# Kernel optimization log

Measured on AMD Instinct MI355X. Metric: run time of the kernel, lower is better.

## Reference

```python
import jax, jax.numpy as jnp
import numpy as np

N_NODES = 50000

def _gcn_layer(x, src, dst, W, b, n_nodes):
    # x: [N, F_in]; src/dst: [E+N] (self-loops already appended)
    h = x @ W  # [N, F_out]
    deg = jax.ops.segment_sum(jnp.ones_like(dst, dtype=h.dtype), dst, num_segments=n_nodes)
    dinv = jnp.where(deg > 0, jax.lax.rsqrt(deg), 0.0)  # deg^{-1/2}
    norm = dinv[src] * dinv[dst]  # [E+N]
    msg = h[src] * norm[:, None]  # gather + scale
    out = jax.ops.segment_sum(msg, dst, num_segments=n_nodes)  # scatter-add
    return out + b

def setup_inputs() -> dict:
    key = jax.random.key(0)
    k1, k2, k3, k4 = jax.random.split(key, 4)
    d = 128
    E = 800000
    x = jax.random.normal(k1, (N_NODES, d), dtype=jnp.float32)
    edge_index = jax.random.randint(k2, (2, E), 0, N_NODES, dtype=jnp.int64)
    W1 = jax.random.normal(k3, (d, d), dtype=jnp.float32) / np.sqrt(d)
    b1 = jnp.zeros((d,), dtype=jnp.float32)
    W2 = jax.random.normal(k4, (d, d), dtype=jnp.float32) / np.sqrt(d)
    b2 = jnp.zeros((d,), dtype=jnp.float32)
    return {"x": x, "edge_index": edge_index, "W1": W1, "b1": b1, "W2": W2, "b2": b2}

def reference(x, edge_index, W1, b1, W2, b2):
    n = x.shape[0]
    loops = jnp.arange(n, dtype=edge_index.dtype)
    src = jnp.concatenate([edge_index[0], loops])  # add self-loops
    dst = jnp.concatenate([edge_index[1], loops])
    h = _gcn_layer(x, src, dst, W1, b1, n)
    h = jax.nn.relu(h)
    z = _gcn_layer(h, src, dst, W2, b2, n)
    return z
```

## Files before the change

kernel.cpp:

```cpp
#include <hip/hip_runtime.h>
#include <hip/hip_fp16.h>

#define NF 128
#define KC 64
#define NPART 4
#define NPMAX 12544

typedef _Float16 half8  __attribute__((ext_vector_type(8)));
typedef _Float16 half4v __attribute__((ext_vector_type(4)));
typedef float    floatx4 __attribute__((ext_vector_type(4)));

__global__ __launch_bounds__(512) void count2_k(
    const int* __restrict__ dst, unsigned char* __restrict__ pcnt,
    int E, int N, int Ec)
{
    __shared__ int lcnt[NPMAX];
    const int p = blockIdx.x & 3, c = blockIdx.x >> 2;
    const int Np = (N + 3) >> 2;
    const int lo = p * Np, hi = min(lo + Np, N);
    const int sz = hi - lo;
    for (int i = threadIdx.x; i < sz; i += 512) lcnt[i] = 0;
    __syncthreads();

    const int e0 = c * Ec, e1 = min(e0 + Ec, E);
    for (int e = e0 + (int)threadIdx.x * 4; e + 3 < e1; e += 512 * 4) {
        int4 d = *(const int4*)(dst + e);
        if (d.x >= lo && d.x < hi) atomicAdd(&lcnt[d.x - lo], 1);
        if (d.y >= lo && d.y < hi) atomicAdd(&lcnt[d.y - lo], 1);
        if (d.z >= lo && d.z < hi) atomicAdd(&lcnt[d.z - lo], 1);
        if (d.w >= lo && d.w < hi) atomicAdd(&lcnt[d.w - lo], 1);
    }
    int rem0 = e0 + ((e1 - e0) & ~3);
    for (int e = rem0 + (int)threadIdx.x; e < e1; e += 512) {
        int d = dst[e];
        if (d >= lo && d < hi) atomicAdd(&lcnt[d - lo], 1);
    }
    __syncthreads();
    for (int i = threadIdx.x; i < sz; i += 512)
        pcnt[(size_t)c * N + lo + i] = (unsigned char)lcnt[i];
}

__global__ __launch_bounds__(256) void pscan2_k(
    unsigned char* __restrict__ pcnt, float* __restrict__ dinv,
    int* __restrict__ rowptr, int* __restrict__ blocksum, int n, int N, int nb,
    const float* __restrict__ W1, const float* __restrict__ W2,
    __half* __restrict__ WT1, __half* __restrict__ WT2)
{
    if ((int)blockIdx.x >= nb) {
        int idx = ((int)blockIdx.x - nb) * 256 + threadIdx.x;
        const float* W = (idx < 16384) ? W1 : W2;
        __half* WT     = (idx < 16384) ? WT1 : WT2;
        int j = idx & 16383;
        int nn = j & 127, k = j >> 7;
        WT[nn * NF + k] = __float2half(W[k * NF + nn]);
        return;
    }
    __shared__ int sm[256];
    int tid = threadIdx.x;
    int bin = blockIdx.x * 256 + tid;
    int total = 0;
    if (bin < n) {
        #pragma unroll 4
        for (int c = 0; c < KC; c++) {
            size_t o = (size_t)c * N + bin;
            int v = pcnt[o];
            pcnt[o] = (unsigned char)total;
            total += v;
        }
        dinv[bin] = rsqrtf((float)total + 1.0f);
    }
    sm[tid] = total;
    __syncthreads();
    #pragma unroll
    for (int d = 1; d < 256; d <<= 1) {
        int t = (tid >= d) ? sm[tid - d] : 0;
        __syncthreads();
        sm[tid] += t;
        __syncthreads();
    }
    if (bin < n) rowptr[bin] = sm[tid] - total;
    if (tid == 255) blocksum[blockIdx.x] = sm[255];
}

template<bool F32IN>
__device__ __forceinline__ void gemm_body512(
    const void* __restrict__ Xv, const __half* __restrict__ WT,
    const float* __restrict__ dinv, __half* __restrict__ out, int M, int bid,
    __half (*wlds)[136])
{
    const int tid = threadIdx.x;
    {
        int r = tid >> 2;
        int c0 = (tid & 3) * 32;
        const half8* s = (const half8*)(WT + (size_t)r * NF + c0);
        half8* d = (half8*)&wlds[r][c0];
        #pragma unroll
        for (int j = 0; j < 4; j++) d[j] = s[j];
    }
    __syncthreads();

    const int wave = tid >> 6, lane = tid & 63;
    const int quad = lane >> 4, l15 = lane & 15;
    const int rowA = bid * 128 + wave * 16 + l15;
    const int rowc = (rowA < M) ? rowA : (M - 1);

    half8 afr[4];
    if (F32IN) {
        const float* X = (const float*)Xv;
        #pragma unroll
        for (int kc = 0; kc < 4; kc++) {
            const floatx4* p = (const floatx4*)(X + (size_t)rowc * NF + kc * 32 + quad * 8);
            floatx4 u = p[0], v = p[1];
            half8 a;
            a[0] = (_Float16)u[0]; a[1] = (_Float16)u[1];
            a[2] = (_Float16)u[2]; a[3] = (_Float16)u[3];
            a[4] = (_Float16)v[0]; a[5] = (_Float16)v[1];
            a[6] = (_Float16)v[2]; a[7] = (_Float16)v[3];
            afr[kc] = a;
        }
    } else {
        const __half* X = (const __half*)Xv;
        #pragma unroll
        for (int kc = 0; kc < 4; kc++)
            afr[kc] = *(const half8*)(X + (size_t)rowc * NF + kc * 32 + quad * 8);
    }

    floatx4 acc[8];
    #pragma unroll
    for (int ct = 0; ct < 8; ct++) { floatx4 z = {0.f, 0.f, 0.f, 0.f}; acc[ct] = z; }

    #pragma unroll
    for (int kc = 0; kc < 4; kc++) {
        #pragma unroll
        for (int ct = 0; ct < 8; ct++) {
            half8 b = *(const half8*)&wlds[ct * 16 + l15][kc * 32 + quad * 8];
            acc[ct] = __builtin_amdgcn_mfma_f32_16x16x32_f16(afr[kc], b, acc[ct], 0, 0, 0);
        }
    }

    const int orow0 = bid * 128 + wave * 16 + quad * 4;
    #pragma unroll
    for (int r = 0; r < 4; r++) {
        int orow = orow0 + r;
        if (orow < M) {
            float s = dinv[orow];
            #pragma unroll
            for (int ct = 0; ct < 8; ct++)
                out[(size_t)orow * NF + ct * 16 + l15] = __float2half(acc[ct][r] * s);
        }
    }
}

__global__ __launch_bounds__(512) void mid_k(
    const int* __restrict__ src, const int* __restrict__ dst,
    const int* __restrict__ rowptr, const unsigned char* __restrict__ coff,
    const int* __restrict__ blocksum, int* __restrict__ rowptr2,
    int* __restrict__ csr, int E, int N, int Ec, int nb,
    const float* __restrict__ X, const __half* __restrict__ WT,
    const float* __restrict__ dinv, __half* __restrict__ H, int GB2)
{
    __shared__ __align__(16) char smem[NPMAX * 4 + 1024];
    const int tid = threadIdx.x;
    if ((int)blockIdx.x < GB2) {
        gemm_body512<true>(X, WT, dinv, H, N, blockIdx.x, (__half(*)[136])smem);
        return;
    }
    int* lcur = (int*)smem;
    int* pref = (int*)(smem + NPMAX * 4);

    const int b = blockIdx.x - GB2;
    const int p = b & 3, c = b >> 2;
    const int Np = (N + 3) >> 2;
    const int lo = p * Np, hi = min(lo + Np, N);
    const int sz = hi - lo;

    int v = (tid < nb) ? blocksum[tid] : 0;
    if (tid < 256) pref[tid] = v;
    __syncthreads();
    #pragma unroll
    for (int d = 1; d < 256; d <<= 1) {
        int t = (tid < 256 && tid >= d) ? pref[tid - d] : 0;
        __syncthreads();
        if (tid < 256) pref[tid] += t;
        __syncthreads();
    }
    if (tid < 256) pref[tid] -= v;
    __syncthreads();

    for (int i = tid; i < sz; i += 512) {
        int bin = lo + i;
        int r = rowptr[bin] + pref[bin >> 8] + (int)coff[(size_t)c * N + bin];
        lcur[i] = r;
        if (c == 0) rowptr2[bin] = r;
    }
    if (c == 0 && p == 0 && tid == 0) rowptr2[N] = E;
    __syncthreads();

    const int e0 = c * Ec, e1 = min(e0 + Ec, E);
    for (int e = e0 + tid * 4; e + 3 < e1; e += 512 * 4) {
        int4 d = *(const int4*)(dst + e);
        int4 s = *(const int4*)(src + e);
        if (d.x >= lo && d.x < hi) csr[atomicAdd(&lcur[d.x - lo], 1)] = s.x;
        if (d.y >= lo && d.y < hi) csr[atomicAdd(&lcur[d.y - lo], 1)] = s.y;
        if (d.z >= lo && d.z < hi) csr[atomicAdd(&lcur[d.z - lo], 1)] = s.z;
        if (d.w >= lo && d.w < hi) csr[atomicAdd(&lcur[d.w - lo], 1)] = s.w;
    }
    int rem0 = e0 + ((e1 - e0) & ~3);
    for (int e = rem0 + tid; e < e1; e += 512) {
        int d = dst[e];
        if (d >= lo && d < hi) csr[atomicAdd(&lcur[d - lo], 1)] = src[e];
    }
}

__device__ __forceinline__ void gather2w(
    const half8* __restrict__ hs8, const int* __restrict__ csr,
    const int* __restrict__ rowptr, int nA, int n,
    int g, int fl, int lane, floatx4& ac0, floatx4& ac1)
{
    const int ep  = g & 1;
    const int isB = g >> 1;
    const int nB  = nA + 1;

    int baseA = 0, cntA = 0, baseB = 0, cntB = 0;
    if (nA < n) {
        baseA = rowptr[nA];
        int mid = rowptr[nA + 1];
        cntA = mid - baseA;
        if (nB < n) { baseB = mid; cntB = rowptr[nB + 1] - mid; }
    }
    const int ccA = min(cntA, 64), ccB = min(cntB, 64);

    int idxA = (lane < ccA) ? __builtin_nontemporal_load(&csr[baseA + lane]) : 0;
    int idxB = (lane < ccB) ? __builtin_nontemporal_load(&csr[baseB + lane]) : 0;

    if (ep == 0) {
        int nd = isB ? nB : nA;
        if (nd < n) {
            half8 s = hs8[(size_t)nd * 16 + fl];
            ac0[0] += (float)s[0]; ac0[1] += (float)s[1];
            ac0[2] += (float)s[2]; ac0[3] += (float)s[3];
            ac1[0] += (float)s[4]; ac1[1] += (float)s[5];
            ac1[2] += (float)s[6]; ac1[3] += (float)s[7];
        }
    }

    const int myc  = isB ? ccB : ccA;
    const int maxc = max(ccA, ccB);
    for (int j = 0; j < maxc; j += 16) {
        int s[8];
        half8 v[8];
        #pragma unroll
        for (int t = 0; t < 8; t++) {
            int e = j + 2 * t + ep;
            int eA = min(e, ccA - 1); eA = (eA < 0) ? 0 : eA;
            int eB = min(e, ccB - 1); eB = (eB < 0) ? 0 : eB;
            int sa = __shfl(idxA, eA, 64);
            int sb = __shfl(idxB, eB, 64);
            s[t] = isB ? sb : sa;
        }
        #pragma unroll
        for (int t = 0; t < 8; t++)
            v[t] = hs8[(size_t)s[t] * 16 + fl];
        #pragma unroll
        for (int t = 0; t < 8; t++) {
            if (j + 2 * t + ep < myc) {
                ac0[0] += (float)v[t][0]; ac0[1] += (float)v[t][1];
                ac0[2] += (float)v[t][2]; ac0[3] += (float)v[t][3];
                ac1[0] += (float)v[t][4]; ac1[1] += (float)v[t][5];
                ac1[2] += (float)v[t][6]; ac1[3] += (float)v[t][7];
            }
        }
    }

    const int cmax = max(cntA, cntB);
    for (int off = 64; off < cmax; off += 64) {
        int cA2 = cntA - off; cA2 = (cA2 < 0) ? 0 : min(cA2, 64);
        int cB2 = cntB - off; cB2 = (cB2 < 0) ? 0 : min(cB2, 64);
        int iA2 = (lane < cA2) ? csr[baseA + off + lane] : 0;
        int iB2 = (lane < cB2) ? csr[baseB + off + lane] : 0;
        int myc2 = isB ? cB2 : cA2;
        int m2   = max(cA2, cB2);
        for (int j = 0; j < m2; j += 16) {
            int s[8];
            half8 v[8];
            #pragma unroll
            for (int t = 0; t < 8; t++) {
                int e = j + 2 * t + ep;
                int eA = min(e, cA2 - 1); eA = (eA < 0) ? 0 : eA;
                int eB = min(e, cB2 - 1); eB = (eB < 0) ? 0 : eB;
                int sa = __shfl(iA2, eA, 64);
                int sb = __shfl(iB2, eB, 64);
                s[t] = isB ? sb : sa;
            }
            #pragma unroll
            for (int t = 0; t < 8; t++)
                v[t] = hs8[(size_t)s[t] * 16 + fl];
            #pragma unroll
            for (int t = 0; t < 8; t++) {
                if (j + 2 * t + ep < myc2) {
                    ac0[0] += (float)v[t][0]; ac0[1] += (float)v[t][1];
                    ac0[2] += (float)v[t][2]; ac0[3] += (float)v[t][3];
                    ac1[0] += (float)v[t][4]; ac1[1] += (float)v[t][5];
                    ac1[2] += (float)v[t][6]; ac1[3] += (float)v[t][7];
                }
            }
        }
    }

    #pragma unroll
    for (int q = 0; q < 4; q++) {
        ac0[q] += __shfl_xor(ac0[q], 16, 64);
        ac1[q] += __shfl_xor(ac1[q], 16, 64);
    }
}

__global__ __launch_bounds__(512) void aggmm_k(
    const __half* __restrict__ hs, const int* __restrict__ rowptr,
    const int* __restrict__ csr, const float* __restrict__ dinv,
    const float* __restrict__ bias, const __half* __restrict__ WT,
    __half* __restrict__ Hout, int n)
{
    __shared__ __half alds[16][136];
    const int tid = threadIdx.x;
    const int wave = tid >> 6, lane = tid & 63;
    const int g = lane >> 4, fl = lane & 15;
    const int nb0 = blockIdx.x * 16;
    const int nA = nb0 + wave * 2;

    floatx4 ac0 = {0.f, 0.f, 0.f, 0.f}, ac1 = {0.f, 0.f, 0.f, 0.f};
    gather2w((const half8*)hs, csr, rowptr, nA, n, g, fl, lane, ac0, ac1);

    if ((g & 1) == 0) {
        int node = nA + (g >> 1);
        int row  = wave * 2 + (g >> 1);
        half8 hv;
        if (node < n) {
            float dv = dinv[node];
            const floatx4 bv0 = *(const floatx4*)&bias[fl * 8];
            const floatx4 bv1 = *(const floatx4*)&bias[fl * 8 + 4];
            hv[0] = (_Float16)fmaxf(dv * ac0[0] + bv0[0], 0.f);
            hv[1] = (_Float16)fmaxf(dv * ac0[1] + bv0[1], 0.f);
            hv[2] = (_Float16)fmaxf(dv * ac0[2] + bv0[2], 0.f);
            hv[3] = (_Float16)fmaxf(dv * ac0[3] + bv0[3], 0.f);
            hv[4] = (_Float16)fmaxf(dv * ac1[0] + bv1[0], 0.f);
            hv[5] = (_Float16)fmaxf(dv * ac1[1] + bv1[1], 0.f);
            hv[6] = (_Float16)fmaxf(dv * ac1[2] + bv1[2], 0.f);
            hv[7] = (_Float16)fmaxf(dv * ac1[3] + bv1[3], 0.f);
        } else {
            #pragma unroll
            for (int i = 0; i < 8; i++) hv[i] = (_Float16)0.f;
        }
        *(half8*)&alds[row][fl * 8] = hv;
    }
    __syncthreads();

    const int quad = lane >> 4, l15 = lane & 15;
    const int ct = wave;
    half8 afr[4];
    #pragma unroll
    for (int kc = 0; kc < 4; kc++)
        afr[kc] = *(const half8*)&alds[l15][kc * 32 + quad * 8];

    floatx4 o0 = {0.f, 0.f, 0.f, 0.f};
    #pragma unroll
    for (int kc = 0; kc < 4; kc++) {
        half8 b = *(const half8*)(WT + (size_t)(ct * 16 + l15) * NF + kc * 32 + quad * 8);
        o0 = __builtin_amdgcn_mfma_f32_16x16x32_f16(afr[kc], b, o0, 0, 0, 0);
    }

    #pragma unroll
    for (int r = 0; r < 4; r++) {
        int node = nb0 + quad * 4 + r;
        if (node < n) {
            float s = dinv[node];
            Hout[(size_t)node * NF + ct * 16 + l15] = __float2half(o0[r] * s);
        }
    }
}

__global__ __launch_bounds__(256) void agg4_k(
    const __half* __restrict__ hs, const int* __restrict__ rowptr,
    const int* __restrict__ csr, const float* __restrict__ dinv,
    const float* __restrict__ bias, float* __restrict__ outf, int n)
{
    const int tid = threadIdx.x;
    const int wave = tid >> 6, lane = tid & 63;
    const int g = lane >> 4, fl = lane & 15;
    const int nA = blockIdx.x * 8 + wave * 2;
    if (nA >= n) return;

    floatx4 ac0 = {0.f, 0.f, 0.f, 0.f}, ac1 = {0.f, 0.f, 0.f, 0.f};
    gather2w((const half8*)hs, csr, rowptr, nA, n, g, fl, lane, ac0, ac1);

    if ((g & 1) == 0) {
        int node = nA + (g >> 1);
        if (node < n) {
            float dv = dinv[node];
            const floatx4 bv0 = *(const floatx4*)&bias[fl * 8];
            const floatx4 bv1 = *(const floatx4*)&bias[fl * 8 + 4];
            floatx4 w0, w1;
            w0[0] = dv * ac0[0] + bv0[0]; w0[1] = dv * ac0[1] + bv0[1];
            w0[2] = dv * ac0[2] + bv0[2]; w0[3] = dv * ac0[3] + bv0[3];
            w1[0] = dv * ac1[0] + bv1[0]; w1[1] = dv * ac1[1] + bv1[1];
            w1[2] = dv * ac1[2] + bv1[2]; w1[3] = dv * ac1[3] + bv1[3];
            *(floatx4*)(outf + (size_t)node * NF + fl * 8)     = w0;
            *(floatx4*)(outf + (size_t)node * NF + fl * 8 + 4) = w1;
        }
    }
}


extern "C" void kernel_launch(void* const* d_in, const int* in_sizes, int n_in,
                              void* d_out, int out_size, void* d_ws, size_t ws_size,
                              hipStream_t stream) {
    const float* x  = (const float*)d_in[0];
    const int*   ei = (const int*)d_in[1];
    const float* W1 = (const float*)d_in[2];
    const float* b1 = (const float*)d_in[3];
    const float* W2 = (const float*)d_in[4];
    const float* b2 = (const float*)d_in[5];
    float* out = (float*)d_out;

    const int N = in_sizes[0] / NF;
    const int E = in_sizes[1] / 2;
    const int* src = ei;
    const int* dst = ei + E;

    char* ws = (char*)d_ws;
    size_t off = 0;
    auto alloc = [&](size_t bytes) {
        void* p = ws + off;
        off += bytes;
        off = (off + 63) & ~(size_t)63;
        return p;
    };
    unsigned char* pcnt = (unsigned char*)alloc((size_t)KC * N);
    int*    rowptr  = (int*)alloc((size_t)(N + 1) * 4);
    int*    rowptr2 = (int*)alloc((size_t)(N + 1) * 4);
    int*    csr     = (int*)alloc((size_t)E * 4);
    float*  dinv    = (float*)alloc((size_t)N * 4);
    int*    bsum    = (int*)alloc((size_t)256 * 4);
    __half* WT1     = (__half*)alloc((size_t)NF * NF * 2);
    __half* WT2     = (__half*)alloc((size_t)NF * NF * 2);
    __half* H16     = (__half*)alloc((size_t)N * NF * 2);
    __half* A16     = (__half*)alloc((size_t)N * NF * 2);

    int nb  = (N + 255) / 256;
    int Ec  = (((E + KC - 1) / KC) + 3) & ~3;
    int GB2 = (N + 127) / 128;
    int fb  = (N + 15) / 16;
    int ab  = (N + 7) / 8;

    count2_k<<<KC * NPART, 512, 0, stream>>>(dst, pcnt, E, N, Ec);
    pscan2_k<<<nb + 128, 256, 0, stream>>>(pcnt, dinv, rowptr, bsum, N, N, nb,
                                           W1, W2, WT1, WT2);
    mid_k<<<GB2 + KC * NPART, 512, 0, stream>>>(src, dst, rowptr, pcnt, bsum,
                                                rowptr2, csr, E, N, Ec, nb,
                                                x, WT1, dinv, H16, GB2);
    aggmm_k<<<fb, 512, 0, stream>>>(H16, rowptr2, csr, dinv, b1, WT2, A16, N);
    agg4_k<<<ab, 256, 0, stream>>>(A16, rowptr2, csr, dinv, b2, out, N);
}
```

Baseline: 204.3 us.

## Replace counting-sort CSR build with fixed-width padded adjacency plus overflow list

Removes the partitioned count, prefix-scan and scatter kernels. Edges now go straight into a padded per-node adjacency of width 64 using global atomics, and any edges past that width go to an overflow list. Degree normalisation is recomputed from the count array instead of a stored dinv. This saves several launches and the scan passes, but adds contended global atomics, a large sparse array, and a linear scan of the overflow list in the aggregation kernels whenever overflow occurs. The GEMM no longer runs fused alongside the scatter, so it now runs after the fill.

```diff
diff --git a/kernel.cpp b/kernel.cpp
--- a/kernel.cpp
+++ b/kernel.cpp
@@ -2,92 +2,68 @@
 #include <hip/hip_fp16.h>
 
 #define NF 128
-#define KC 64
-#define NPART 4
-#define NPMAX 12544
+#define DMAX 64
 
 typedef _Float16 half8  __attribute__((ext_vector_type(8)));
 typedef _Float16 half4v __attribute__((ext_vector_type(4)));
 typedef float    floatx4 __attribute__((ext_vector_type(4)));
 
-__global__ __launch_bounds__(512) void count2_k(
-    const int* __restrict__ dst, unsigned char* __restrict__ pcnt,
-    int E, int N, int Ec)
-{
-    __shared__ int lcnt[NPMAX];
-    const int p = blockIdx.x & 3, c = blockIdx.x >> 2;
-    const int Np = (N + 3) >> 2;
-    const int lo = p * Np, hi = min(lo + Np, N);
-    const int sz = hi - lo;
-    for (int i = threadIdx.x; i < sz; i += 512) lcnt[i] = 0;
-    __syncthreads();
-
-    const int e0 = c * Ec, e1 = min(e0 + Ec, E);
-    for (int e = e0 + (int)threadIdx.x * 4; e + 3 < e1; e += 512 * 4) {
-        int4 d = *(const int4*)(dst + e);
-        if (d.x >= lo && d.x < hi) atomicAdd(&lcnt[d.x - lo], 1);
-        if (d.y >= lo && d.y < hi) atomicAdd(&lcnt[d.y - lo], 1);
-        if (d.z >= lo && d.z < hi) atomicAdd(&lcnt[d.z - lo], 1);
-        if (d.w >= lo && d.w < hi) atomicAdd(&lcnt[d.w - lo], 1);
-    }
-    int rem0 = e0 + ((e1 - e0) & ~3);
-    for (int e = rem0 + (int)threadIdx.x; e < e1; e += 512) {
-        int d = dst[e];
-        if (d >= lo && d < hi) atomicAdd(&lcnt[d - lo], 1);
-    }
-    __syncthreads();
-    for (int i = threadIdx.x; i < sz; i += 512)
-        pcnt[(size_t)c * N + lo + i] = (unsigned char)lcnt[i];
-}
-
-__global__ __launch_bounds__(256) void pscan2_k(
-    unsigned char* __restrict__ pcnt, float* __restrict__ dinv,
-    int* __restrict__ rowptr, int* __restrict__ blocksum, int n, int N, int nb,
+__global__ __launch_bounds__(256) void z_k(
+    int* __restrict__ cnt, int N, int zb,
     const float* __restrict__ W1, const float* __restrict__ W2,
     __half* __restrict__ WT1, __half* __restrict__ WT2)
 {
-    if ((int)blockIdx.x >= nb) {
-        int idx = ((int)blockIdx.x - nb) * 256 + threadIdx.x;
-        const float* W = (idx < 16384) ? W1 : W2;
-        __half* WT     = (idx < 16384) ? WT1 : WT2;
-        int j = idx & 16383;
-        int nn = j & 127, k = j >> 7;
-        WT[nn * NF + k] = __float2half(W[k * NF + nn]);
+    int b = blockIdx.x;
+    if (b < zb) {
+        int i = b * 256 + threadIdx.x;
+        if (i <= N) cnt[i] = 0;
         return;
     }
-    __shared__ int sm[256];
-    int tid = threadIdx.x;
-    int bin = blockIdx.x * 256 + tid;
-    int total = 0;
-    if (bin < n) {
-        #pragma unroll 4
-        for (int c = 0; c < KC; c++) {
-            size_t o = (size_t)c * N + bin;
-            int v = pcnt[o];
-            pcnt[o] = (unsigned char)total;
-            total += v;
-        }
-        dinv[bin] = rsqrtf((float)total + 1.0f);
-    }
-    sm[tid] = total;
-    __syncthreads();
-    #pragma unroll
-    for (int d = 1; d < 256; d <<= 1) {
-        int t = (tid >= d) ? sm[tid - d] : 0;
-        __syncthreads();
-        sm[tid] += t;
-        __syncthreads();
-    }
-    if (bin < n) rowptr[bin] = sm[tid] - total;
-    if (tid == 255) blocksum[blockIdx.x] = sm[255];
-}
-
-template<bool F32IN>
-__device__ __forceinline__ void gemm_body512(
-    const void* __restrict__ Xv, const __half* __restrict__ WT,
-    const float* __restrict__ dinv, __half* __restrict__ out, int M, int bid,
-    __half (*wlds)[136])
-{
+    int idx = (b - zb) * 256 + threadIdx.x;
+    const float* W = (idx < 16384) ? W1 : W2;
+    __half* WT     = (idx < 16384) ? WT1 : WT2;
+    int j = idx & 16383;
+    int nn = j & 127, k = j >> 7;
+    WT[nn * NF + k] = __float2half(W[k * NF + nn]);
+}
+
+__device__ __forceinline__ void fill_one(
+    int d, int s, int* __restrict__ cnt, int* __restrict__ csrF,
+    int* __restrict__ ovf, int N)
+{
+    int pos = atomicAdd(&cnt[d], 1);
+    if (pos < DMAX) {
+        csrF[(size_t)d * DMAX + pos] = s;
+    } else {
+        int o = atomicAdd(&cnt[N], 1);
+        ovf[2 * o] = d; ovf[2 * o + 1] = s;
+    }
+}
+
+__global__ __launch_bounds__(256) void fill_k(
+    const int* __restrict__ src, const int* __restrict__ dst,
+    int* __restrict__ cnt, int* __restrict__ csrF, int* __restrict__ ovf,
+    int E, int N)
+{
+    int i4 = (blockIdx.x * 256 + threadIdx.x) * 4;
+    if (i4 + 3 < E) {
+        int4 d = *(const int4*)(dst + i4);
+        int4 s = *(const int4*)(src + i4);
+        fill_one(d.x, s.x, cnt, csrF, ovf, N);
+        fill_one(d.y, s.y, cnt, csrF, ovf, N);
+        fill_one(d.z, s.z, cnt, csrF, ovf, N);
+        fill_one(d.w, s.w, cnt, csrF, ovf, N);
+    } else {
+        for (int e = i4; e < E; e++)
+            fill_one(dst[e], src[e], cnt, csrF, ovf, N);
+    }
+}
+
+__global__ __launch_bounds__(512) void gemm1_k(
+    const float* __restrict__ X, const __half* __restrict__ WT,
+    const int* __restrict__ cnt, __half* __restrict__ H, int M)
+{
+    __shared__ __half wlds[128][136];
     const int tid = threadIdx.x;
     {
         int r = tid >> 2;
@@ -101,28 +77,20 @@
 
     const int wave = tid >> 6, lane = tid & 63;
     const int quad = lane >> 4, l15 = lane & 15;
-    const int rowA = bid * 128 + wave * 16 + l15;
+    const int rowA = blockIdx.x * 128 + wave * 16 + l15;
     const int rowc = (rowA < M) ? rowA : (M - 1);
 
     half8 afr[4];
-    if (F32IN) {
-        const float* X = (const float*)Xv;
-        #pragma unroll
-        for (int kc = 0; kc < 4; kc++) {
-            const floatx4* p = (const floatx4*)(X + (size_t)rowc * NF + kc * 32 + quad * 8);
-            floatx4 u = p[0], v = p[1];
-            half8 a;
-            a[0] = (_Float16)u[0]; a[1] = (_Float16)u[1];
-            a[2] = (_Float16)u[2]; a[3] = (_Float16)u[3];
-            a[4] = (_Float16)v[0]; a[5] = (_Float16)v[1];
-            a[6] = (_Float16)v[2]; a[7] = (_Float16)v[3];
-            afr[kc] = a;
-        }
-    } else {
-        const __half* X = (const __half*)Xv;
-        #pragma unroll
-        for (int kc = 0; kc < 4; kc++)
-            afr[kc] = *(const half8*)(X + (size_t)rowc * NF + kc * 32 + quad * 8);
+    #pragma unroll
+    for (int kc = 0; kc < 4; kc++) {
+        const floatx4* p = (const floatx4*)(X + (size_t)rowc * NF + kc * 32 + quad * 8);
+        floatx4 u = p[0], v = p[1];
+        half8 a;
+        a[0] = (_Float16)u[0]; a[1] = (_Float16)u[1];
+        a[2] = (_Float16)u[2]; a[3] = (_Float16)u[3];
+        a[4] = (_Float16)v[0]; a[5] = (_Float16)v[1];
+        a[6] = (_Float16)v[2]; a[7] = (_Float16)v[3];
+        afr[kc] = a;
     }
 
     floatx4 acc[8];
@@ -138,100 +106,35 @@
         }
     }
 
-    const int orow0 = bid * 128 + wave * 16 + quad * 4;
+    const int orow0 = blockIdx.x * 128 + wave * 16 + quad * 4;
     #pragma unroll
     for (int r = 0; r < 4; r++) {
         int orow = orow0 + r;
         if (orow < M) {
-            float s = dinv[orow];
+            float dv = rsqrtf((float)cnt[orow] + 1.0f);
             #pragma unroll
             for (int ct = 0; ct < 8; ct++)
-                out[(size_t)orow * NF + ct * 16 + l15] = __float2half(acc[ct][r] * s);
-        }
-    }
-}
-
-__global__ __launch_bounds__(512) void mid_k(
-    const int* __restrict__ src, const int* __restrict__ dst,
-    const int* __restrict__ rowptr, const unsigned char* __restrict__ coff,
-    const int* __restrict__ blocksum, int* __restrict__ rowptr2,
-    int* __restrict__ csr, int E, int N, int Ec, int nb,
-    const float* __restrict__ X, const __half* __restrict__ WT,
-    const float* __restrict__ dinv, __half* __restrict__ H, int GB2)
-{
-    __shared__ __align__(16) char smem[NPMAX * 4 + 1024];
-    const int tid = threadIdx.x;
-    if ((int)blockIdx.x < GB2) {
-        gemm_body512<true>(X, WT, dinv, H, N, blockIdx.x, (__half(*)[136])smem);
-        return;
-    }
-    int* lcur = (int*)smem;
-    int* pref = (int*)(smem + NPMAX * 4);
-
-    const int b = blockIdx.x - GB2;
-    const int p = b & 3, c = b >> 2;
-    const int Np = (N + 3) >> 2;
-    const int lo = p * Np, hi = min(lo + Np, N);
-    const int sz = hi - lo;
-
-    int v = (tid < nb) ? blocksum[tid] : 0;
-    if (tid < 256) pref[tid] = v;
-    __syncthreads();
-    #pragma unroll
-    for (int d = 1; d < 256; d <<= 1) {
-        int t = (tid < 256 && tid >= d) ? pref[tid - d] : 0;
-        __syncthreads();
-        if (tid < 256) pref[tid] += t;
-        __syncthreads();
-    }
-    if (tid < 256) pref[tid] -= v;
-    __syncthreads();
-
-    for (int i = tid; i < sz; i += 512) {
-        int bin = lo + i;
-        int r = rowptr[bin] + pref[bin >> 8] + (int)coff[(size_t)c * N + bin];
-        lcur[i] = r;
-        if (c == 0) rowptr2[bin] = r;
-    }
-    if (c == 0 && p == 0 && tid == 0) rowptr2[N] = E;
-    __syncthreads();
-
-    const int e0 = c * Ec, e1 = min(e0 + Ec, E);
-    for (int e = e0 + tid * 4; e + 3 < e1; e += 512 * 4) {
-        int4 d = *(const int4*)(dst + e);
-        int4 s = *(const int4*)(src + e);
-        if (d.x >= lo && d.x < hi) csr[atomicAdd(&lcur[d.x - lo], 1)] = s.x;
-        if (d.y >= lo && d.y < hi) csr[atomicAdd(&lcur[d.y - lo], 1)] = s.y;
-        if (d.z >= lo && d.z < hi) csr[atomicAdd(&lcur[d.z - lo], 1)] = s.z;
-        if (d.w >= lo && d.w < hi) csr[atomicAdd(&lcur[d.w - lo], 1)] = s.w;
-    }
-    int rem0 = e0 + ((e1 - e0) & ~3);
-    for (int e = rem0 + tid; e < e1; e += 512) {
-        int d = dst[e];
-        if (d >= lo && d < hi) csr[atomicAdd(&lcur[d - lo], 1)] = src[e];
+                H[(size_t)orow * NF + ct * 16 + l15] = __float2half(acc[ct][r] * dv);
+        }
     }
 }
 
 __device__ __forceinline__ void gather2w(
-    const half8* __restrict__ hs8, const int* __restrict__ csr,
-    const int* __restrict__ rowptr, int nA, int n,
-    int g, int fl, int lane, floatx4& ac0, floatx4& ac1)
+    const half8* __restrict__ hs8, const int* __restrict__ csrF,
+    const int* __restrict__ cnt, int nA, int n,
+    int g, int fl, int lane, floatx4& ac0, floatx4& ac1,
+    const int* __restrict__ ovf, int novf)
 {
     const int ep  = g & 1;
     const int isB = g >> 1;
     const int nB  = nA + 1;
 
-    int baseA = 0, cntA = 0, baseB = 0, cntB = 0;
-    if (nA < n) {
-        baseA = rowptr[nA];
-        int mid = rowptr[nA + 1];
-        cntA = mid - baseA;
-        if (nB < n) { baseB = mid; cntB = rowptr[nB + 1] - mid; }
-    }
-    const int ccA = min(cntA, 64), ccB = min(cntB, 64);
-
-    int idxA = (lane < ccA) ? __builtin_nontemporal_load(&csr[baseA + lane]) : 0;
-    int idxB = (lane < ccB) ? __builtin_nontemporal_load(&csr[baseB + lane]) : 0;
+    int cntA = (nA < n) ? cnt[nA] : 0;
+    int cntB = (nB < n) ? cnt[nB] : 0;
+    const int ccA = min(cntA, DMAX), ccB = min(cntB, DMAX);
+
+    int idxA = (lane < ccA) ? __builtin_nontemporal_load(&csrF[(size_t)nA * DMAX + lane]) : 0;
+    int idxB = (lane < ccB) ? __builtin_nontemporal_load(&csrF[(size_t)nB * DMAX + lane]) : 0;
 
     if (ep == 0) {
         int nd = isB ? nB : nA;
@@ -272,37 +175,16 @@
         }
     }
 
-    const int cmax = max(cntA, cntB);
-    for (int off = 64; off < cmax; off += 64) {
-        int cA2 = cntA - off; cA2 = (cA2 < 0) ? 0 : min(cA2, 64);
-        int cB2 = cntB - off; cB2 = (cB2 < 0) ? 0 : min(cB2, 64);
-        int iA2 = (lane < cA2) ? csr[baseA + off + lane] : 0;
-        int iB2 = (lane < cB2) ? csr[baseB + off + lane] : 0;
-        int myc2 = isB ? cB2 : cA2;
-        int m2   = max(cA2, cB2);
-        for (int j = 0; j < m2; j += 16) {
-            int s[8];
-            half8 v[8];
-            #pragma unroll
-            for (int t = 0; t < 8; t++) {
-                int e = j + 2 * t + ep;
-                int eA = min(e, cA2 - 1); eA = (eA < 0) ? 0 : eA;
-                int eB = min(e, cB2 - 1); eB = (eB < 0) ? 0 : eB;
-                int sa = __shfl(iA2, eA, 64);
-                int sb = __shfl(iB2, eB, 64);
-                s[t] = isB ? sb : sa;
-            }
-            #pragma unroll
-            for (int t = 0; t < 8; t++)
-                v[t] = hs8[(size_t)s[t] * 16 + fl];
-            #pragma unroll
-            for (int t = 0; t < 8; t++) {
-                if (j + 2 * t + ep < myc2) {
-                    ac0[0] += (float)v[t][0]; ac0[1] += (float)v[t][1];
-                    ac0[2] += (float)v[t][2]; ac0[3] += (float)v[t][3];
-                    ac1[0] += (float)v[t][4]; ac1[1] += (float)v[t][5];
-                    ac1[2] += (float)v[t][6]; ac1[3] += (float)v[t][7];
-                }
+    if (novf > 0 && ep == 0) {
+        int myN = isB ? nB : nA;
+        for (int i = 0; i < novf; i++) {
+            int d = ovf[2 * i];
+            if (d == myN) {
+                half8 v = hs8[(size_t)ovf[2 * i + 1] * 16 + fl];
+                ac0[0] += (float)v[0]; ac0[1] += (float)v[1];
+                ac0[2] += (float)v[2]; ac0[3] += (float)v[3];
+                ac1[0] += (float)v[4]; ac1[1] += (float)v[5];
+                ac1[2] += (float)v[6]; ac1[3] += (float)v[7];
             }
         }
     }
@@ -315,10 +197,10 @@
 }
 
 __global__ __launch_bounds__(512) void aggmm_k(
-    const __half* __restrict__ hs, const int* __restrict__ rowptr,
-    const int* __restrict__ csr, const float* __restrict__ dinv,
-    const float* __restrict__ bias, const __half* __restrict__ WT,
-    __half* __restrict__ Hout, int n)
+    const __half* __restrict__ hs, const int* __restrict__ csrF,
+    const int* __restrict__ cnt, const float* __restrict__ bias,
+    const __half* __restrict__ WT, __half* __restrict__ Hout, int n,
+    const int* __restrict__ ovf)
 {
     __shared__ __half alds[16][136];
     const int tid = threadIdx.x;
@@ -326,16 +208,17 @@
     const int g = lane >> 4, fl = lane & 15;
     const int nb0 = blockIdx.x * 16;
     const int nA = nb0 + wave * 2;
+    const int novf = cnt[n];
 
     floatx4 ac0 = {0.f, 0.f, 0.f, 0.f}, ac1 = {0.f, 0.f, 0.f, 0.f};
-    gather2w((const half8*)hs, csr, rowptr, nA, n, g, fl, lane, ac0, ac1);
+    gather2w((const half8*)hs, csrF, cnt, nA, n, g, fl, lane, ac0, ac1, ovf, novf);
 
     if ((g & 1) == 0) {
         int node = nA + (g >> 1);
         int row  = wave * 2 + (g >> 1);
         half8 hv;
         if (node < n) {
-            float dv = dinv[node];
+            float dv = rsqrtf((float)cnt[node] + 1.0f);
             const floatx4 bv0 = *(const floatx4*)&bias[fl * 8];
             const floatx4 bv1 = *(const floatx4*)&bias[fl * 8 + 4];
             hv[0] = (_Float16)fmaxf(dv * ac0[0] + bv0[0], 0.f);
@@ -372,30 +255,31 @@
     for (int r = 0; r < 4; r++) {
         int node = nb0 + quad * 4 + r;
         if (node < n) {
-            float s = dinv[node];
-            Hout[(size_t)node * NF + ct * 16 + l15] = __float2half(o0[r] * s);
+            float dv = rsqrtf((float)cnt[node] + 1.0f);
+            Hout[(size_t)node * NF + ct * 16 + l15] = __float2half(o0[r] * dv);
         }
     }
 }
 
 __global__ __launch_bounds__(256) void agg4_k(
-    const __half* __restrict__ hs, const int* __restrict__ rowptr,
-    const int* __restrict__ csr, const float* __restrict__ dinv,
-    const float* __restrict__ bias, float* __restrict__ outf, int n)
+    const __half* __restrict__ hs, const int* __restrict__ csrF,
+    const int* __restrict__ cnt, const float* __restrict__ bias,
+    float* __restrict__ outf, int n, const int* __restrict__ ovf)
 {
     const int tid = threadIdx.x;
     const int wave = tid >> 6, lane = tid & 63;
     const int g = lane >> 4, fl = lane & 15;
     const int nA = blockIdx.x * 8 + wave * 2;
     if (nA >= n) return;
+    const int novf = cnt[n];
 
     floatx4 ac0 = {0.f, 0.f, 0.f, 0.f}, ac1 = {0.f, 0.f, 0.f, 0.f};
-    gather2w((const half8*)hs, csr, rowptr, nA, n, g, fl, lane, ac0, ac1);
+    gather2w((const half8*)hs, csrF, cnt, nA, n, g, fl, lane, ac0, ac1, ovf, novf);
 
     if ((g & 1) == 0) {
         int node = nA + (g >> 1);
         if (node < n) {
-            float dv = dinv[node];
+            float dv = rsqrtf((float)cnt[node] + 1.0f);
             const floatx4 bv0 = *(const floatx4*)&bias[fl * 8];
             const floatx4 bv1 = *(const floatx4*)&bias[fl * 8 + 4];
             floatx4 w0, w1;
@@ -434,29 +318,23 @@
         off = (off + 63) & ~(size_t)63;
         return p;
     };
-    unsigned char* pcnt = (unsigned char*)alloc((size_t)KC * N);
-    int*    rowptr  = (int*)alloc((size_t)(N + 1) * 4);
-    int*    rowptr2 = (int*)alloc((size_t)(N + 1) * 4);
-    int*    csr     = (int*)alloc((size_t)E * 4);
-    float*  dinv    = (float*)alloc((size_t)N * 4);
-    int*    bsum    = (int*)alloc((size_t)256 * 4);
-    __half* WT1     = (__half*)alloc((size_t)NF * NF * 2);
-    __half* WT2     = (__half*)alloc((size_t)NF * NF * 2);
-    __half* H16     = (__half*)alloc((size_t)N * NF * 2);
-    __half* A16     = (__half*)alloc((size_t)N * NF * 2);
-
-    int nb  = (N + 255) / 256;
-    int Ec  = (((E + KC - 1) / KC) + 3) & ~3;
-    int GB2 = (N + 127) / 128;
-    int fb  = (N + 15) / 16;
+    int*    cnt  = (int*)alloc((size_t)(N + 1) * 4);
+    int*    csrF = (int*)alloc((size_t)N * DMAX * 4);
+    int*    ovf  = (int*)alloc((size_t)E * 2 * 4);
+    __half* WT1  = (__half*)alloc((size_t)NF * NF * 2);
+    __half* WT2  = (__half*)alloc((size_t)NF * NF * 2);
+    __half* H16  = (__half*)alloc((size_t)N * NF * 2);
+    __half* A16  = (__half*)alloc((size_t)N * NF * 2);
+
+    int zb = (N + 1 + 255) / 256;
+    int fbF = (E + 1023) / 1024;
+    int GB  = (N + 127) / 128;
+    int mb  = (N + 15) / 16;
     int ab  = (N + 7) / 8;
 
-    count2_k<<<KC * NPART, 512, 0, stream>>>(dst, pcnt, E, N, Ec);
-    pscan2_k<<<nb + 128, 256, 0, stream>>>(pcnt, dinv, rowptr, bsum, N, N, nb,
-                                           W1, W2, WT1, WT2);
-    mid_k<<<GB2 + KC * NPART, 512, 0, stream>>>(src, dst, rowptr, pcnt, bsum,
-                                                rowptr2, csr, E, N, Ec, nb,
-                                                x, WT1, dinv, H16, GB2);
-    aggmm_k<<<fb, 512, 0, stream>>>(H16, rowptr2, csr, dinv, b1, WT2, A16, N);
-    agg4_k<<<ab, 256, 0, stream>>>(A16, rowptr2, csr, dinv, b2, out, N);
-}
+    z_k<<<zb + 128, 256, 0, stream>>>(cnt, N, zb, W1, W2, WT1, WT2);
+    fill_k<<<fbF, 256, 0, stream>>>(src, dst, cnt, csrF, ovf, E, N);
+    gemm1_k<<<GB, 512, 0, stream>>>(x, WT1, cnt, H16, N);
+    aggmm_k<<<mb, 512, 0, stream>>>(H16, csrF, cnt, b1, WT2, A16, N, ovf);
+    agg4_k<<<ab, 256, 0, stream>>>(A16, csrF, cnt, b2, out, N, ovf);
+}
```

Result: slower. 210.8 us (+3.2%).
